# Kernel optimization log

Hardware: AMD Instinct MI355X
Metric: run time of the kernel (lower is better)

## Reference

```python
import jax, jax.numpy as jnp
import numpy as np
from jax import lax

EPS = 1e-12  # torch F.normalize eps


def _l2norm(x):
    n = jnp.linalg.norm(x, axis=-1, keepdims=True)
    return x / jnp.maximum(n, EPS)


def _conv1x1(x, w):
    # x: [B,C,H,W], w: [O,C] (1x1 conv, no bias)
    return jnp.einsum('bchw,oc->bohw', x, w)


def _se(x, w1, w2):
    # AdaptiveAvgPool2d(1) -> 1x1 conv (no bias) -> ReLU -> 1x1 conv (no bias) -> ReLU
    p = jnp.mean(x, axis=(2, 3))                      # [B,256]
    h = jax.nn.relu(jnp.einsum('bc,oc->bo', p, w1))   # [B,320]
    return jax.nn.relu(jnp.einsum('bc,oc->bo', h, w2))  # [B,1280]


def _tdec(x, wk_w, wk_b, wv_w, wv_b, red_w, rise_w, rise_b):
    # fc_reduce: 1x1 conv 256->128
    x1 = _conv1x1(x, red_w)                           # [B,128,H,W]
    B, d, H, W = x1.shape
    t = x1.reshape(B, d, H * W).transpose(0, 2, 1)    # [B,N,128] tokens
    # same WK linear produces both q and k (xq == xk in the source)
    k = _l2norm(jnp.einsum('bnd,ed->bne', t, wk_w) + wk_b)  # [B,N,128]
    v = _l2norm(jnp.einsum('bnd,ed->bne', t, wv_w) + wv_b)  # [B,N,128]
    # bmm(wq[B,d,N], wk[B,N,d]) -> [B,d,d] channel gram, temp 30 softmax
    attn = jax.nn.softmax(jnp.einsum('bni,bnj->bij', k, k) * 30.0, axis=-1)
    # bmm(attn[B,d,d], v^T[B,d,N]) -> [B,d,N], reshape back to map
    ot = jnp.einsum('bij,bnj->bin', attn, v).reshape(B, d, H, W)
    return _conv1x1(ot, rise_w) + rise_b[None, :, None, None]


def _fwd(x0, x1, x2, x3, x4, spec_w1, spec_w2, comm_w1, comm_w2,
         pre_w, pre_b, wk1_w, wk1_b, wv1_w, wv1_b, red1_w, rise1_w, rise1_b,
         wk2_w, wk2_b, wv2_w, wv2_b, red2_w, rise2_w, rise2_b):
    xs = jnp.stack([x0, x1, x2, x3, x4])              # [5,B,256,H,W]
    B = x0.shape[0]
    # reduce(lambda x,y: abs(x-y), down_x)
    diff = x0
    for xi in (x1, x2, x3, x4):
        diff = jnp.abs(diff - xi)
    ssum = xs.sum(axis=0)
    wd = jax.nn.softmax(_se(diff, spec_w1, spec_w2).reshape(B, 5, 256), axis=1)
    ws = jax.nn.softmax(_se(ssum, comm_w1, comm_w2).reshape(B, 5, 256), axis=1)
    # v2[i] = x_i*wd_i + x_i*ws_i + x_i ; v3 = sum_i v2[i]
    v3 = jnp.einsum('sbchw,bsc->bchw', xs, wd + ws + 1.0)
    pre = jax.nn.relu(
        lax.conv_general_dilated(v3, pre_w, (1, 1), ((1, 1), (1, 1)),
                                 dimension_numbers=('NCHW', 'OIHW', 'NCHW'))
        + pre_b[None, :, None, None])
    f1 = _tdec(pre, wk1_w, wk1_b, wv1_w, wv1_b, red1_w, rise1_w, rise1_b)
    f3 = _tdec(f1 + v3, wk2_w, wk2_b, wv2_w, wv2_b, red2_w, rise2_w, rise2_b)
    return f1 + f3 + v3


def setup_inputs() -> dict:
    key = jax.random.key(0)
    ks = iter(jax.random.split(key, 40))
    B, C, H, W = 16, 256, 64, 64

    def p(shape, scale=0.05):
        return jax.random.normal(next(ks), shape, jnp.float32) * scale

    inp = {f'x{i}': jax.random.normal(next(ks), (B, C, H, W), jnp.float32) for i in range(5)}
    inp.update(
        spec_w1=p((320, 256)), spec_w2=p((1280, 320)),
        comm_w1=p((320, 256)), comm_w2=p((1280, 320)),
        pre_w=p((256, 256, 3, 3)), pre_b=p((256,)),
        wk1_w=p((128, 128)), wk1_b=p((128,)), wv1_w=p((128, 128)), wv1_b=p((128,)),
        red1_w=p((128, 256)), rise1_w=p((256, 128)), rise1_b=p((256,)),
        wk2_w=p((128, 128)), wk2_b=p((128,)), wv2_w=p((128, 128)), wv2_b=p((128,)),
        red2_w=p((128, 256)), rise2_w=p((256, 128)), rise2_b=p((256,)),
    )
    return inp


def reference(x0, x1, x2, x3, x4, spec_w1, spec_w2, comm_w1, comm_w2,
              pre_w, pre_b, wk1_w, wk1_b, wv1_w, wv1_b, red1_w, rise1_w, rise1_b,
              wk2_w, wk2_b, wv2_w, wv2_b, red2_w, rise2_w, rise2_b):
    return _fwd(x0, x1, x2, x3, x4, spec_w1, spec_w2, comm_w1, comm_w2,
                pre_w, pre_b, wk1_w, wk1_b, wv1_w, wv1_b, red1_w, rise1_w, rise1_b,
                wk2_w, wk2_b, wv2_w, wv2_b, red2_w, rise2_w, rise2_b)
```

## Files before the change

### kernel.cpp

```cpp
#include <hip/hip_runtime.h>

#define DI __device__ __forceinline__

typedef short s16x8 __attribute__((ext_vector_type(8)));
typedef unsigned short u16;
typedef u16 u16x8 __attribute__((ext_vector_type(8)));
typedef u16 u16x16 __attribute__((ext_vector_type(16)));
typedef float f32x4 __attribute__((ext_vector_type(4)));

DI float bf2f(u16 v) { return __builtin_bit_cast(float, (unsigned)v << 16); }
DI u16 f2bf(float f) {
  unsigned u = __builtin_bit_cast(unsigned, f);
  return (u16)((u + 0x7fffu + ((u >> 16) & 1u)) >> 16);
}

__global__ void k_cast(u16* __restrict__ dst, const float* __restrict__ src, int n) {
  int i = blockIdx.x * 256 + threadIdx.x;
  if (i < n) dst[i] = f2bf(src[i]);
}

__global__ void k_wconv(u16* __restrict__ dst, const float* __restrict__ src) {
  int i = blockIdx.x * 256 + threadIdx.x;
  if (i < 9 * 256 * 256) {
    int tap = i >> 16, rem = i & 65535;
    dst[i] = f2bf(src[(size_t)rem * 9 + tap]);
  }
}

__global__ __launch_bounds__(256) void k_pool(
    const float* __restrict__ x0, const float* __restrict__ x1,
    const float* __restrict__ x2, const float* __restrict__ x3,
    const float* __restrict__ x4, float* __restrict__ pd, float* __restrict__ ps) {
  int c = blockIdx.x, b = blockIdx.y;
  size_t base = ((size_t)b * 256 + c) * 4096;
  float sd = 0.f, sm = 0.f;
  for (int p = threadIdx.x; p < 4096; p += 256) {
    float a0 = x0[base + p], a1 = x1[base + p], a2 = x2[base + p];
    float a3 = x3[base + p], a4 = x4[base + p];
    float d = fabsf(a0 - a1); d = fabsf(d - a2); d = fabsf(d - a3); d = fabsf(d - a4);
    sd += d; sm += a0 + a1 + a2 + a3 + a4;
  }
  for (int o = 32; o; o >>= 1) { sd += __shfl_xor(sd, o); sm += __shfl_xor(sm, o); }
  __shared__ float rb[4][2];
  int wv = threadIdx.x >> 6, lane = threadIdx.x & 63;
  if (!lane) { rb[wv][0] = sd; rb[wv][1] = sm; }
  __syncthreads();
  if (!threadIdx.x) {
    float a = rb[0][0] + rb[1][0] + rb[2][0] + rb[3][0];
    float s2 = rb[0][1] + rb[1][1] + rb[2][1] + rb[3][1];
    pd[b * 256 + c] = a * (1.f / 4096.f);
    ps[b * 256 + c] = s2 * (1.f / 4096.f);
  }
}

__global__ __launch_bounds__(256) void k_se1(
    const float* __restrict__ pd, const float* __restrict__ ps,
    const float* __restrict__ sw1, const float* __restrict__ cw1,
    float* __restrict__ h1) {
  int b = blockIdx.y, z = blockIdx.z;
  int wv = threadIdx.x >> 6, lane = threadIdx.x & 63;
  int e = blockIdx.x * 4 + wv;
  const float* in = (z ? ps : pd) + b * 256;
  const float* w = (z ? cw1 : sw1) + (size_t)e * 256;
  float a = 0.f;
#pragma unroll
  for (int i = 0; i < 4; ++i) a += in[lane + 64 * i] * w[lane + 64 * i];
  for (int o = 32; o; o >>= 1) a += __shfl_xor(a, o);
  if (!lane) h1[((size_t)z * 16 + b) * 320 + e] = fmaxf(a, 0.f);
}

__global__ __launch_bounds__(256) void k_se2(
    const float* __restrict__ h1, const float* __restrict__ sw2,
    const float* __restrict__ cw2, float* __restrict__ h2) {
  int b = blockIdx.y, z = blockIdx.z;
  int wv = threadIdx.x >> 6, lane = threadIdx.x & 63;
  int e = blockIdx.x * 4 + wv;
  const float* in = h1 + ((size_t)z * 16 + b) * 320;
  const float* w = (z ? cw2 : sw2) + (size_t)e * 320;
  float a = 0.f;
#pragma unroll
  for (int i = 0; i < 5; ++i) a += in[lane + 64 * i] * w[lane + 64 * i];
  for (int o = 32; o; o >>= 1) a += __shfl_xor(a, o);
  if (!lane) h2[((size_t)z * 16 + b) * 1280 + e] = fmaxf(a, 0.f);
}

__global__ __launch_bounds__(256) void k_se3(
    const float* __restrict__ h2, float* __restrict__ wt) {
  int b = blockIdx.x, t = threadIdx.x;
  const float* Hs = h2 + (size_t)b * 1280;
  const float* Hc = h2 + (size_t)(16 + b) * 1280;
  float d0 = Hs[t], d1 = Hs[256 + t], d2 = Hs[512 + t], d3 = Hs[768 + t], d4 = Hs[1024 + t];
  float m = fmaxf(fmaxf(fmaxf(d0, d1), fmaxf(d2, d3)), d4);
  float e0 = expf(d0 - m), e1 = expf(d1 - m), e2 = expf(d2 - m), e3 = expf(d3 - m), e4 = expf(d4 - m);
  float inv = 1.f / (e0 + e1 + e2 + e3 + e4);
  float c0 = Hc[t], c1 = Hc[256 + t], c2 = Hc[512 + t], c3 = Hc[768 + t], c4 = Hc[1024 + t];
  float mc = fmaxf(fmaxf(fmaxf(c0, c1), fmaxf(c2, c3)), c4);
  float g0 = expf(c0 - mc), g1 = expf(c1 - mc), g2 = expf(c2 - mc), g3 = expf(c3 - mc), g4 = expf(c4 - mc);
  float ci = 1.f / (g0 + g1 + g2 + g3 + g4);
  size_t base = (size_t)b * 1280 + t;
  wt[base + 0 * 256] = e0 * inv + g0 * ci + 1.f;
  wt[base + 1 * 256] = e1 * inv + g1 * ci + 1.f;
  wt[base + 2 * 256] = e2 * inv + g2 * ci + 1.f;
  wt[base + 3 * 256] = e3 * inv + g3 * ci + 1.f;
  wt[base + 4 * 256] = e4 * inv + g4 * ci + 1.f;
}

__global__ __launch_bounds__(256) void k_v3(
    const float* __restrict__ x0, const float* __restrict__ x1,
    const float* __restrict__ x2, const float* __restrict__ x3,
    const float* __restrict__ x4, const float* __restrict__ wt,
    u16* __restrict__ v3b) {
  int h = blockIdx.x, b = blockIdx.y;
  __shared__ float W[1280];
  for (int s = threadIdx.x; s < 1280; s += 256) W[s] = wt[(size_t)b * 1280 + s];
  __syncthreads();
  int t = threadIdx.x, w = t >> 2, oct = t & 3;
  size_t pbase = ((size_t)b * 256) * 4096 + h * 64 + w;
  size_t obase = ((size_t)b * 4096 + h * 64 + w) * 256;
  for (int pass = 0; pass < 8; ++pass) {
    int c0 = oct * 8 + pass * 32;
    u16x8 ov;
#pragma unroll
    for (int jj = 0; jj < 8; ++jj) {
      int c = c0 + jj;
      size_t a = pbase + (size_t)c * 4096;
      float s = x0[a] * W[c] + x1[a] * W[256 + c] + x2[a] * W[512 + c] +
                x3[a] * W[768 + c] + x4[a] * W[1024 + c];
      ov[jj] = f2bf(s);
    }
    *(u16x8*)(v3b + obase + c0) = ov;
  }
}

__global__ __launch_bounds__(256) void k_conv(
    const u16* __restrict__ v3b, const u16* __restrict__ Wt,
    const float* __restrict__ bias, u16* __restrict__ pre) {
  int o = blockIdx.x;
  int wg = (o & 7) * 128 + (o >> 3);
  int oh = wg & 1, hp = (wg >> 1) & 31, b = wg >> 6;
  __shared__ __align__(16) u16 Ain[4 * 66 * 40];
  __shared__ __align__(16) u16 Bld[2][128 * 40];
  int t = threadIdx.x, wv = t >> 6, lane = t & 63;
  int wm = (wv >> 1) * 64, wn = (wv & 1) * 64, fr = lane & 15, ko = lane >> 4;

  auto loadA = [&](int cc, int s) -> u16x16 {
    int r = s >> 7, rest = s & 127, w = rest >> 1, half = rest & 1;
    int hs = hp * 2 - 1 + r;
    u16x16 v = {};
    if ((unsigned)hs < 64u)
      v = *(const u16x16*)(v3b + (((size_t)b * 64 + hs) * 64 + w) * 256 + cc * 32 + half * 16);
    return v;
  };
  auto storeA = [&](int s, u16x16 v) {
    int r = s >> 7, rest = s & 127, w = rest >> 1, half = rest & 1;
    *(u16x16*)(Ain + (r * 66 + w + 1) * 40 + half * 16) = v;
  };
  auto loadB = [&](int tap, int cc) -> u16x16 {
    int n = t >> 1, half = t & 1;
    return *(const u16x16*)(Wt + ((size_t)tap * 256 + oh * 128 + n) * 256 + cc * 32 + half * 16);
  };
  auto storeB = [&](int bsel, u16x16 v) {
    int n = t >> 1, half = t & 1;
    *(u16x16*)(Bld[bsel] + n * 40 + half * 16) = v;
  };

  for (int s = t; s < 320; s += 256) {
    int r = s / 80, rem = s % 80;
    int col = (rem >= 40) ? 65 : 0, c = rem % 40;
    Ain[(r * 66 + col) * 40 + c] = 0;
  }
  storeA(t, loadA(0, t));
  storeA(t + 256, loadA(0, t + 256));
  storeB(0, loadB(0, 0));
  __syncthreads();

  f32x4 acc[4][4] = {};
  int buf = 0;
  for (int cc = 0; cc < 8; ++cc) {
#pragma unroll
    for (int tap = 0; tap < 9; ++tap) {
      u16x16 pA0, pA1, pB;
      bool doA = false, doB = false;
      if (tap < 8) {
        doB = true;
        pB = loadB(tap + 1, cc);
      } else if (cc < 7) {
        doA = true; doB = true;
        pB = loadB(0, cc + 1);
        pA0 = loadA(cc + 1, t);
        pA1 = loadA(cc + 1, t + 256);
      }
      const int dh = tap / 3 - 1, dw = tap % 3 - 1;
      s16x8 af[4], bfr[4];
#pragma unroll
      for (int i = 0; i < 4; ++i) {
        int m = wm + i * 16 + fr, r = m >> 6, wq = m & 63;
        af[i] = *(const s16x8*)(Ain + ((r + dh + 1) * 66 + (wq + dw + 1)) * 40 + ko * 8);
      }
#pragma unroll
      for (int j = 0; j < 4; ++j)
        bfr[j] = *(const s16x8*)(Bld[buf] + (wn + j * 16 + fr) * 40 + ko * 8);
#pragma unroll
      for (int i = 0; i < 4; ++i)
#pragma unroll
        for (int j = 0; j < 4; ++j)
          acc[i][j] = __builtin_amdgcn_mfma_f32_16x16x32_bf16(af[i], bfr[j], acc[i][j], 0, 0, 0);
      if (doA) __syncthreads();
      if (doB) storeB(buf ^ 1, pB);
      if (doA) { storeA(t, pA0); storeA(t + 256, pA1); }
      __syncthreads();
      buf ^= 1;
    }
  }
#pragma unroll
  for (int i = 0; i < 4; ++i) {
    int m0 = wm + i * 16 + ko * 4;
#pragma unroll
    for (int j = 0; j < 4; ++j) {
      int och = oh * 128 + wn + j * 16 + fr;
      float bv = bias[och];
#pragma unroll
      for (int r = 0; r < 4; ++r) {
        float v = fmaxf(acc[i][j][r] + bv, 0.f);
        pre[((size_t)b * 4096 + hp * 128 + m0 + r) * 256 + och] = f2bf(v);
      }
    }
  }
}

template <int MODE>
__global__ __launch_bounds__(256) void k_gemm(
    const u16* __restrict__ A, int lda, const u16* __restrict__ B0,
    const u16* __restrict__ B1, int ldb, int K,
    const float* __restrict__ bias0, const float* __restrict__ bias1,
    u16* __restrict__ out0, u16* __restrict__ out1,
    const u16* __restrict__ add0, const u16* __restrict__ add1,
    float* __restrict__ outf) {
  int nt = blockIdx.x, b = blockIdx.y, z = blockIdx.z;
  const u16* Ab = A + ((size_t)b * 4096 + nt * 128) * (size_t)lda;
  const u16* Bb;
  if constexpr (MODE == 1) Bb = (z ? B1 : B0);
  else if constexpr (MODE == 2) Bb = B0 + (size_t)b * 128 * ldb;
  else Bb = B0 + (size_t)z * 128 * ldb;
  __shared__ __align__(16) u16 Ald[128 * 40];
  __shared__ __align__(16) u16 Bld[128 * 40];
  int t = threadIdx.x, wv = t >> 6, lane = t & 63;
  int wm = (wv >> 1) * 64, wn = (wv & 1) * 64, fr = lane & 15, ko = lane >> 4;
  f32x4 acc[4][4] = {};
  for (int kc = 0; kc < K; kc += 32) {
    for (int s = t; s < 512; s += 256) {
      int r = s >> 2, ks = s & 3;
      *(u16x8*)(Ald + r * 40 + ks * 8) = *(const u16x8*)(Ab + (size_t)r * lda + kc + ks * 8);
    }
    for (int s = t; s < 512; s += 256) {
      int r = s >> 2, ks = s & 3;
      *(u16x8*)(Bld + r * 40 + ks * 8) = *(const u16x8*)(Bb + (size_t)r * ldb + kc + ks * 8);
    }
    __syncthreads();
    s16x8 af[4], bf[4];
#pragma unroll
    for (int i = 0; i < 4; ++i) af[i] = *(const s16x8*)(Ald + (wm + i * 16 + fr) * 40 + ko * 8);
#pragma unroll
    for (int j = 0; j < 4; ++j) bf[j] = *(const s16x8*)(Bld + (wn + j * 16 + fr) * 40 + ko * 8);
#pragma unroll
    for (int i = 0; i < 4; ++i)
#pragma unroll
      for (int j = 0; j < 4; ++j)
        acc[i][j] = __builtin_amdgcn_mfma_f32_16x16x32_bf16(af[i], bf[j], acc[i][j], 0, 0, 0);
    __syncthreads();
  }
  size_t tokbase = (size_t)b * 4096 + nt * 128;
#pragma unroll
  for (int i = 0; i < 4; ++i) {
    int m0 = wm + i * 16 + ko * 4;
#pragma unroll
    for (int j = 0; j < 4; ++j) {
      int nc = wn + j * 16 + fr;
      if constexpr (MODE == 0 || MODE == 2) {
        u16* dst = out0 + (tokbase + m0) * 128 + nc;
#pragma unroll
        for (int r = 0; r < 4; ++r) dst[(size_t)r * 128] = f2bf(acc[i][j][r]);
      } else if constexpr (MODE == 1) {
        float bv = (z ? bias1 : bias0)[nc];
        u16* dst = (z ? out1 : out0) + (tokbase + m0) * 128 + nc;
#pragma unroll
        for (int r = 0; r < 4; ++r) dst[(size_t)r * 128] = f2bf(acc[i][j][r] + bv);
      } else if constexpr (MODE == 3) {
        int o = z * 128 + nc;
        float bv = bias0[o];
        size_t idx = (tokbase + m0) * 256 + o;
#pragma unroll
        for (int r = 0; r < 4; ++r) {
          float f1v = acc[i][j][r] + bv;
          out0[idx + (size_t)r * 256] = f2bf(f1v);
          out1[idx + (size_t)r * 256] = f2bf(f1v + bf2f(add0[idx + (size_t)r * 256]));
        }
      } else {
        int o = z * 128 + nc;
        float bv = bias0[o];
        size_t idx = (tokbase + m0) * 256 + o;
        f32x4 vv;
#pragma unroll
        for (int r = 0; r < 4; ++r)
          vv[r] = acc[i][j][r] + bv + bf2f(add0[idx + (size_t)r * 256]) + bf2f(add1[idx + (size_t)r * 256]);
        *(f32x4*)(outf + ((size_t)b * 256 + o) * 4096 + nt * 128 + m0) = vv;
      }
    }
  }
}

__global__ __launch_bounds__(256) void k_norm(const u16* __restrict__ kraw,
                                              u16* __restrict__ ktout,
                                              u16* __restrict__ vbuf) {
  int nt = blockIdx.x, b = blockIdx.y, kind = blockIdx.z;
  int t = threadIdx.x, r = t >> 2, q = t & 3;
  __shared__ __align__(16) u16 T[128 * 72];
  size_t row = (size_t)b * 4096 + nt * 64 + r;
  const u16* src = (kind ? (const u16*)vbuf : kraw) + row * 128 + q * 32;
  float vals[32];
  float ss = 0.f;
#pragma unroll
  for (int s = 0; s < 4; ++s) {
    u16x8 v8 = *(const u16x8*)(src + s * 8);
#pragma unroll
    for (int e = 0; e < 8; ++e) { float f = bf2f(v8[e]); vals[s * 8 + e] = f; ss += f * f; }
  }
  ss += __shfl_xor(ss, 1);
  ss += __shfl_xor(ss, 2);
  float sc = 1.f / fmaxf(sqrtf(ss), 1e-12f);
  if (kind) {
    u16* dst = vbuf + row * 128 + q * 32;
#pragma unroll
    for (int s = 0; s < 4; ++s) {
      u16x8 o8;
#pragma unroll
      for (int e = 0; e < 8; ++e) o8[e] = f2bf(vals[s * 8 + e] * sc);
      *(u16x8*)(dst + s * 8) = o8;
    }
  } else {
#pragma unroll
    for (int s = 0; s < 4; ++s)
#pragma unroll
      for (int e = 0; e < 8; ++e)
        T[(q * 32 + s * 8 + e) * 72 + r] = f2bf(vals[s * 8 + e] * sc);
    __syncthreads();
    for (int s2 = t; s2 < 1024; s2 += 256) {
      int i = s2 >> 3, sg = s2 & 7;
      *(u16x8*)(ktout + ((size_t)b * 128 + i) * 4096 + nt * 64 + sg * 8) =
          *(const u16x8*)(T + i * 72 + sg * 8);
    }
  }
}

__global__ __launch_bounds__(256) void k_gram(const u16* __restrict__ kt, float* __restrict__ gp) {
  int ks = blockIdx.x, b = blockIdx.y;
  const u16* base = kt + (size_t)b * 128 * 4096 + ks * 256;
  __shared__ __align__(16) u16 Tld[128 * 40];
  int t = threadIdx.x, wv = t >> 6, lane = t & 63;
  int wm = (wv >> 1) * 64, wn = (wv & 1) * 64, fr = lane & 15, ko = lane >> 4;
  f32x4 acc[4][4] = {};
  for (int kc = 0; kc < 256; kc += 32) {
    for (int s = t; s < 512; s += 256) {
      int r = s >> 2, k2 = s & 3;
      *(u16x8*)(Tld + r * 40 + k2 * 8) = *(const u16x8*)(base + (size_t)r * 4096 + kc + k2 * 8);
    }
    __syncthreads();
    s16x8 af[4], bf[4];
#pragma unroll
    for (int i = 0; i < 4; ++i) af[i] = *(const s16x8*)(Tld + (wm + i * 16 + fr) * 40 + ko * 8);
#pragma unroll
    for (int j = 0; j < 4; ++j) bf[j] = *(const s16x8*)(Tld + (wn + j * 16 + fr) * 40 + ko * 8);
#pragma unroll
    for (int i = 0; i < 4; ++i)
#pragma unroll
      for (int j = 0; j < 4; ++j)
        acc[i][j] = __builtin_amdgcn_mfma_f32_16x16x32_bf16(af[i], bf[j], acc[i][j], 0, 0, 0);
    __syncthreads();
  }
  float* dst = gp + ((size_t)(ks * 16 + b) * 128) * 128;
#pragma unroll
  for (int i = 0; i < 4; ++i) {
    int m0 = wm + i * 16 + ko * 4;
#pragma unroll
    for (int j = 0; j < 4; ++j) {
      int nc = wn + j * 16 + fr;
#pragma unroll
      for (int r = 0; r < 4; ++r) dst[(size_t)(m0 + r) * 128 + nc] = acc[i][j][r];
    }
  }
}

__global__ void k_soft(const float* __restrict__ gp, u16* __restrict__ attn) {
  int i = blockIdx.x, b = blockIdx.y, l = threadIdx.x;
  float s0 = 0.f, s1 = 0.f;
  for (int ks = 0; ks < 16; ++ks) {
    const float* row = gp + (((size_t)ks * 16 + b) * 128 + i) * 128;
    s0 += row[l]; s1 += row[l + 64];
  }
  s0 *= 30.f; s1 *= 30.f;
  float m = fmaxf(s0, s1);
  for (int o = 32; o; o >>= 1) m = fmaxf(m, __shfl_xor(m, o));
  float e0 = expf(s0 - m), e1 = expf(s1 - m);
  float s = e0 + e1;
  for (int o = 32; o; o >>= 1) s += __shfl_xor(s, o);
  float inv = 1.f / s;
  u16* dst = attn + ((size_t)b * 128 + i) * 128;
  dst[l] = f2bf(e0 * inv);
  dst[l + 64] = f2bf(e1 * inv);
}

extern "C" void kernel_launch(void* const* d_in, const int* in_sizes, int n_in,
                              void* d_out, int out_size, void* d_ws, size_t ws_size,
                              hipStream_t stream) {
  (void)in_sizes; (void)n_in; (void)out_size; (void)ws_size;
  const float* x0 = (const float*)d_in[0];
  const float* x1 = (const float*)d_in[1];
  const float* x2 = (const float*)d_in[2];
  const float* x3 = (const float*)d_in[3];
  const float* x4 = (const float*)d_in[4];
  const float* spec_w1 = (const float*)d_in[5];
  const float* spec_w2 = (const float*)d_in[6];
  const float* comm_w1 = (const float*)d_in[7];
  const float* comm_w2 = (const float*)d_in[8];
  const float* pre_w = (const float*)d_in[9];
  const float* pre_bias = (const float*)d_in[10];
  const float* wk1_w = (const float*)d_in[11];
  const float* wk1_b = (const float*)d_in[12];
  const float* wv1_w = (const float*)d_in[13];
  const float* wv1_b = (const float*)d_in[14];
  const float* red1_w = (const float*)d_in[15];
  const float* rise1_w = (const float*)d_in[16];
  const float* rise1_b = (const float*)d_in[17];
  const float* wk2_w = (const float*)d_in[18];
  const float* wk2_b = (const float*)d_in[19];
  const float* wv2_w = (const float*)d_in[20];
  const float* wv2_b = (const float*)d_in[21];
  const float* red2_w = (const float*)d_in[22];
  const float* rise2_w = (const float*)d_in[23];
  const float* rise2_b = (const float*)d_in[24];
  float* out = (float*)d_out;

  char* wsp = (char*)d_ws;
  size_t off = 0;
  auto alloc = [&](size_t bytes) -> void* {
    off = (off + 255) & ~(size_t)255;
    void* p = wsp + off;
    off += bytes;
    return p;
  };
  float* pd = (float*)alloc(16 * 256 * 4);
  float* ps = (float*)alloc(16 * 256 * 4);
  float* h1b = (float*)alloc(2 * 16 * 320 * 4);
  float* h2b = (float*)alloc(2 * 16 * 1280 * 4);
  float* wtb = (float*)alloc(16 * 5 * 256 * 4);
  u16* v3b = (u16*)alloc((size_t)16 * 4096 * 256 * 2);
  u16* Wtc = (u16*)alloc((size_t)9 * 256 * 256 * 2);
  u16* red1b = (u16*)alloc(128 * 256 * 2);
  u16* wk1b = (u16*)alloc(128 * 128 * 2);
  u16* wv1b = (u16*)alloc(128 * 128 * 2);
  u16* rise1b = (u16*)alloc(256 * 128 * 2);
  u16* red2b = (u16*)alloc(128 * 256 * 2);
  u16* wk2b = (u16*)alloc(128 * 128 * 2);
  u16* wv2b = (u16*)alloc(128 * 128 * 2);
  u16* rise2b = (u16*)alloc(256 * 128 * 2);
  u16* pre = (u16*)alloc((size_t)16 * 4096 * 256 * 2);
  u16* tbuf = (u16*)alloc((size_t)16 * 4096 * 128 * 2);
  u16* kraw = (u16*)alloc((size_t)16 * 4096 * 128 * 2);
  u16* khat = (u16*)alloc((size_t)16 * 4096 * 128 * 2);
  u16* vbuf = (u16*)alloc((size_t)16 * 4096 * 128 * 2);
  u16* attn = (u16*)alloc((size_t)16 * 128 * 128 * 2);
  u16* Obuf = (u16*)alloc((size_t)16 * 4096 * 128 * 2);
  u16* f1b = (u16*)alloc((size_t)16 * 4096 * 256 * 2);
  float* gpart = (float*)tbuf;
  u16* in2b = pre;

  k_cast<<<dim3(128), 256, 0, stream>>>(red1b, red1_w, 32768);
  k_cast<<<dim3(64), 256, 0, stream>>>(wk1b, wk1_w, 16384);
  k_cast<<<dim3(64), 256, 0, stream>>>(wv1b, wv1_w, 16384);
  k_cast<<<dim3(128), 256, 0, stream>>>(rise1b, rise1_w, 32768);
  k_cast<<<dim3(128), 256, 0, stream>>>(red2b, red2_w, 32768);
  k_cast<<<dim3(64), 256, 0, stream>>>(wk2b, wk2_w, 16384);
  k_cast<<<dim3(64), 256, 0, stream>>>(wv2b, wv2_w, 16384);
  k_cast<<<dim3(128), 256, 0, stream>>>(rise2b, rise2_w, 32768);
  k_wconv<<<dim3(2304), 256, 0, stream>>>(Wtc, pre_w);

  k_pool<<<dim3(256, 16), 256, 0, stream>>>(x0, x1, x2, x3, x4, pd, ps);
  k_se1<<<dim3(80, 16, 2), 256, 0, stream>>>(pd, ps, spec_w1, comm_w1, h1b);
  k_se2<<<dim3(320, 16, 2), 256, 0, stream>>>(h1b, spec_w2, comm_w2, h2b);
  k_se3<<<dim3(16), 256, 0, stream>>>(h2b, wtb);
  k_v3<<<dim3(64, 16), 256, 0, stream>>>(x0, x1, x2, x3, x4, wtb, v3b);
  k_conv<<<dim3(1024), 256, 0, stream>>>(v3b, Wtc, pre_bias, pre);

  k_gemm<0><<<dim3(32, 16, 1), 256, 0, stream>>>(pre, 256, red1b, nullptr, 256, 256,
      nullptr, nullptr, tbuf, nullptr, nullptr, nullptr, nullptr);
  k_gemm<1><<<dim3(32, 16, 2), 256, 0, stream>>>(tbuf, 128, wk1b, wv1b, 128, 128,
      wk1_b, wv1_b, kraw, vbuf, nullptr, nullptr, nullptr);
  k_norm<<<dim3(64, 16, 2), 256, 0, stream>>>(kraw, khat, vbuf);
  k_gram<<<dim3(16, 16), 256, 0, stream>>>(khat, gpart);
  k_soft<<<dim3(128, 16), 64, 0, stream>>>(gpart, attn);
  k_gemm<2><<<dim3(32, 16, 1), 256, 0, stream>>>(vbuf, 128, attn, nullptr, 128, 128,
      nullptr, nullptr, Obuf, nullptr, nullptr, nullptr, nullptr);
  k_gemm<3><<<dim3(32, 16, 2), 256, 0, stream>>>(Obuf, 128, rise1b, nullptr, 128, 128,
      rise1_b, nullptr, f1b, in2b, v3b, nullptr, nullptr);

  k_gemm<0><<<dim3(32, 16, 1), 256, 0, stream>>>(in2b, 256, red2b, nullptr, 256, 256,
      nullptr, nullptr, tbuf, nullptr, nullptr, nullptr, nullptr);
  k_gemm<1><<<dim3(32, 16, 2), 256, 0, stream>>>(tbuf, 128, wk2b, wv2b, 128, 128,
      wk2_b, wv2_b, kraw, vbuf, nullptr, nullptr, nullptr);
  k_norm<<<dim3(64, 16, 2), 256, 0, stream>>>(kraw, khat, vbuf);
  k_gram<<<dim3(16, 16), 256, 0, stream>>>(khat, gpart);
  k_soft<<<dim3(128, 16), 64, 0, stream>>>(gpart, attn);
  k_gemm<2><<<dim3(32, 16, 1), 256, 0, stream>>>(vbuf, 128, attn, nullptr, 128, 128,
      nullptr, nullptr, Obuf, nullptr, nullptr, nullptr, nullptr);
  k_gemm<4><<<dim3(32, 16, 2), 256, 0, stream>>>(Obuf, 128, rise2b, nullptr, 128, 128,
      rise2_b, nullptr, nullptr, nullptr, f1b, v3b, out);
}
```

Before: 536.6 us.

## Fuse reduce, QKV projection and L2-norm into one kernel; restage v3 transpose

Replaces the separate reduce GEMM, K/V projection GEMM and normalisation kernels with one k_qkv kernel. It keeps the reduced tokens in shared memory, applies the bias and L2 norm in registers, and writes khat already transposed. This removes the round trips of tbuf and kraw through global memory and two launches per attention block. Separately, k_v3 now reads the inputs coalesced along width and transposes through shared memory, and the eight weight-cast launches are merged into one. The fused kernel uses more shared memory and issues its K and V projections serially inside each block, with grid size 32x16 instead of 32x16x2.

```diff
diff --git a/kernel.cpp b/kernel.cpp
--- a/kernel.cpp
+++ b/kernel.cpp
@@ -14,9 +14,22 @@
   return (u16)((u + 0x7fffu + ((u >> 16) & 1u)) >> 16);
 }
 
-__global__ void k_cast(u16* __restrict__ dst, const float* __restrict__ src, int n) {
+__global__ void k_cast8(u16* __restrict__ dst,
+    const float* __restrict__ s0, const float* __restrict__ s1,
+    const float* __restrict__ s2, const float* __restrict__ s3,
+    const float* __restrict__ s4, const float* __restrict__ s5,
+    const float* __restrict__ s6, const float* __restrict__ s7) {
   int i = blockIdx.x * 256 + threadIdx.x;
-  if (i < n) dst[i] = f2bf(src[i]);
+  const float* src; int base;
+  if (i < 32768) { src = s0; base = 0; }
+  else if (i < 49152) { src = s1; base = 32768; }
+  else if (i < 65536) { src = s2; base = 49152; }
+  else if (i < 98304) { src = s3; base = 65536; }
+  else if (i < 131072) { src = s4; base = 98304; }
+  else if (i < 147456) { src = s5; base = 131072; }
+  else if (i < 163840) { src = s6; base = 147456; }
+  else { src = s7; base = 163840; }
+  dst[i] = f2bf(src[i - base]);
 }
 
 __global__ void k_wconv(u16* __restrict__ dst, const float* __restrict__ src) {
@@ -112,22 +125,27 @@
     u16* __restrict__ v3b) {
   int h = blockIdx.x, b = blockIdx.y;
   __shared__ float W[1280];
-  for (int s = threadIdx.x; s < 1280; s += 256) W[s] = wt[(size_t)b * 1280 + s];
+  __shared__ u16 T[256][72];
+  int t = threadIdx.x, wv = t >> 6, l = t & 63;
+  for (int s = t; s < 1280; s += 256) W[s] = wt[(size_t)b * 1280 + s];
   __syncthreads();
-  int t = threadIdx.x, w = t >> 2, oct = t & 3;
-  size_t pbase = ((size_t)b * 256) * 4096 + h * 64 + w;
+  size_t rowbase = (size_t)b * 256 * 4096 + h * 64 + l;
+#pragma unroll 4
+  for (int k = 0; k < 64; ++k) {
+    int c = wv * 64 + k;
+    size_t a = rowbase + (size_t)c * 4096;
+    float s = x0[a] * W[c] + x1[a] * W[256 + c] + x2[a] * W[512 + c] +
+              x3[a] * W[768 + c] + x4[a] * W[1024 + c];
+    T[c][l] = f2bf(s);
+  }
+  __syncthreads();
+  int w = t >> 2, oct = t & 3;
   size_t obase = ((size_t)b * 4096 + h * 64 + w) * 256;
   for (int pass = 0; pass < 8; ++pass) {
     int c0 = oct * 8 + pass * 32;
     u16x8 ov;
 #pragma unroll
-    for (int jj = 0; jj < 8; ++jj) {
-      int c = c0 + jj;
-      size_t a = pbase + (size_t)c * 4096;
-      float s = x0[a] * W[c] + x1[a] * W[256 + c] + x2[a] * W[512 + c] +
-                x3[a] * W[768 + c] + x4[a] * W[1024 + c];
-      ov[jj] = f2bf(s);
-    }
+    for (int jj = 0; jj < 8; ++jj) ov[jj] = T[c0 + jj][w];
     *(u16x8*)(v3b + obase + c0) = ov;
   }
 }
@@ -228,6 +246,159 @@
   }
 }
 
+__global__ __launch_bounds__(256) void k_qkv(
+    const u16* __restrict__ in,
+    const u16* __restrict__ redW,
+    const u16* __restrict__ wkW,
+    const u16* __restrict__ wvW,
+    const float* __restrict__ kb, const float* __restrict__ vb,
+    u16* __restrict__ vout,
+    u16* __restrict__ khat) {
+  int nt = blockIdx.x, b = blockIdx.y;
+  const u16* Ab = in + ((size_t)b * 4096 + nt * 128) * 256;
+  __shared__ __align__(16) u16 Ald[128 * 40];
+  __shared__ __align__(16) u16 Bld[128 * 40];
+  __shared__ __align__(16) u16 T[128 * 136];
+  __shared__ float SS[2][128];
+  int t = threadIdx.x, wv = t >> 6, lane = t & 63;
+  int wm = (wv >> 1) * 64, wn = (wv & 1) * 64, fr = lane & 15, ko = lane >> 4;
+  f32x4 acc[4][4] = {};
+  for (int kc = 0; kc < 256; kc += 32) {
+    for (int s = t; s < 512; s += 256) {
+      int r = s >> 2, ks = s & 3;
+      *(u16x8*)(Ald + r * 40 + ks * 8) = *(const u16x8*)(Ab + (size_t)r * 256 + kc + ks * 8);
+    }
+    for (int s = t; s < 512; s += 256) {
+      int r = s >> 2, ks = s & 3;
+      *(u16x8*)(Bld + r * 40 + ks * 8) = *(const u16x8*)(redW + (size_t)r * 256 + kc + ks * 8);
+    }
+    __syncthreads();
+    s16x8 af[4], bf[4];
+#pragma unroll
+    for (int i = 0; i < 4; ++i) af[i] = *(const s16x8*)(Ald + (wm + i * 16 + fr) * 40 + ko * 8);
+#pragma unroll
+    for (int j = 0; j < 4; ++j) bf[j] = *(const s16x8*)(Bld + (wn + j * 16 + fr) * 40 + ko * 8);
+#pragma unroll
+    for (int i = 0; i < 4; ++i)
+#pragma unroll
+      for (int j = 0; j < 4; ++j)
+        acc[i][j] = __builtin_amdgcn_mfma_f32_16x16x32_bf16(af[i], bf[j], acc[i][j], 0, 0, 0);
+    __syncthreads();
+  }
+#pragma unroll
+  for (int i = 0; i < 4; ++i)
+#pragma unroll
+    for (int j = 0; j < 4; ++j)
+#pragma unroll
+      for (int r = 0; r < 4; ++r)
+        T[(wm + i * 16 + ko * 4 + r) * 136 + wn + j * 16 + fr] = f2bf(acc[i][j][r]);
+
+  for (int z = 0; z < 2; ++z) {
+    const u16* W = z ? wkW : wvW;
+    const float* bias = z ? kb : vb;
+    f32x4 a2[4][4] = {};
+#pragma unroll
+    for (int h = 0; h < 2; ++h) {
+      __syncthreads();
+      for (int s = t; s < 512; s += 256) {
+        int r = s >> 2, ks = s & 3;
+        *(u16x8*)(Ald + r * 40 + ks * 8) = *(const u16x8*)(W + (size_t)r * 128 + h * 64 + ks * 8);
+      }
+      for (int s = t; s < 512; s += 256) {
+        int r = s >> 2, ks = s & 3;
+        *(u16x8*)(Bld + r * 40 + ks * 8) = *(const u16x8*)(W + (size_t)r * 128 + h * 64 + 32 + ks * 8);
+      }
+      __syncthreads();
+#pragma unroll
+      for (int kk = 0; kk < 2; ++kk) {
+        const u16* Bsrc = kk ? Bld : Ald;
+        s16x8 af[4], bf[4];
+#pragma unroll
+        for (int i = 0; i < 4; ++i)
+          af[i] = *(const s16x8*)(T + (size_t)(wm + i * 16 + fr) * 136 + h * 64 + kk * 32 + ko * 8);
+#pragma unroll
+        for (int j = 0; j < 4; ++j)
+          bf[j] = *(const s16x8*)(Bsrc + (wn + j * 16 + fr) * 40 + ko * 8);
+#pragma unroll
+        for (int i = 0; i < 4; ++i)
+#pragma unroll
+          for (int j = 0; j < 4; ++j)
+            a2[i][j] = __builtin_amdgcn_mfma_f32_16x16x32_bf16(af[i], bf[j], a2[i][j], 0, 0, 0);
+      }
+    }
+    float bj[4];
+#pragma unroll
+    for (int j = 0; j < 4; ++j) bj[j] = bias[wn + j * 16 + fr];
+    float pss[4][4];
+#pragma unroll
+    for (int i = 0; i < 4; ++i)
+#pragma unroll
+      for (int r = 0; r < 4; ++r) pss[i][r] = 0.f;
+#pragma unroll
+    for (int i = 0; i < 4; ++i)
+#pragma unroll
+      for (int j = 0; j < 4; ++j)
+#pragma unroll
+        for (int r = 0; r < 4; ++r) {
+          float v = a2[i][j][r] + bj[j];
+          a2[i][j][r] = v;
+          pss[i][r] += v * v;
+        }
+#pragma unroll
+    for (int m = 1; m < 16; m <<= 1)
+#pragma unroll
+      for (int i = 0; i < 4; ++i)
+#pragma unroll
+        for (int r = 0; r < 4; ++r) pss[i][r] += __shfl_xor(pss[i][r], m);
+    if (fr == 0)
+#pragma unroll
+      for (int i = 0; i < 4; ++i)
+#pragma unroll
+        for (int r = 0; r < 4; ++r) SS[wv & 1][wm + i * 16 + ko * 4 + r] = pss[i][r];
+    __syncthreads();
+    float sc[4][4];
+#pragma unroll
+    for (int i = 0; i < 4; ++i)
+#pragma unroll
+      for (int r = 0; r < 4; ++r) {
+        int tok = wm + i * 16 + ko * 4 + r;
+        float s2 = SS[0][tok] + SS[1][tok];
+        sc[i][r] = 1.f / fmaxf(sqrtf(s2), 1e-12f);
+      }
+#pragma unroll
+    for (int i = 0; i < 4; ++i)
+#pragma unroll
+      for (int j = 0; j < 4; ++j)
+#pragma unroll
+        for (int r = 0; r < 4; ++r) a2[i][j][r] *= sc[i][r];
+    if (z == 0) {
+      size_t tokbase = (size_t)b * 4096 + nt * 128;
+#pragma unroll
+      for (int i = 0; i < 4; ++i)
+#pragma unroll
+        for (int j = 0; j < 4; ++j) {
+          u16* dst = vout + (tokbase + wm + i * 16 + ko * 4) * 128 + wn + j * 16 + fr;
+#pragma unroll
+          for (int r = 0; r < 4; ++r) dst[(size_t)r * 128] = f2bf(a2[i][j][r]);
+        }
+    } else {
+#pragma unroll
+      for (int i = 0; i < 4; ++i)
+#pragma unroll
+        for (int j = 0; j < 4; ++j)
+#pragma unroll
+          for (int r = 0; r < 4; ++r)
+            T[(size_t)(wn + j * 16 + fr) * 136 + wm + i * 16 + ko * 4 + r] = f2bf(a2[i][j][r]);
+      __syncthreads();
+      for (int s = t; s < 2048; s += 256) {
+        int ch = s >> 4, sg = s & 15;
+        *(u16x8*)(khat + ((size_t)b * 128 + ch) * 4096 + nt * 128 + sg * 8) =
+            *(const u16x8*)(T + ch * 136 + sg * 8);
+      }
+    }
+  }
+}
+
 template <int MODE>
 __global__ __launch_bounds__(256) void k_gemm(
     const u16* __restrict__ A, int lda, const u16* __restrict__ B0,
@@ -239,8 +410,7 @@
   int nt = blockIdx.x, b = blockIdx.y, z = blockIdx.z;
   const u16* Ab = A + ((size_t)b * 4096 + nt * 128) * (size_t)lda;
   const u16* Bb;
-  if constexpr (MODE == 1) Bb = (z ? B1 : B0);
-  else if constexpr (MODE == 2) Bb = B0 + (size_t)b * 128 * ldb;
+  if constexpr (MODE == 2) Bb = B0 + (size_t)b * 128 * ldb;
   else Bb = B0 + (size_t)z * 128 * ldb;
   __shared__ __align__(16) u16 Ald[128 * 40];
   __shared__ __align__(16) u16 Bld[128 * 40];
@@ -276,15 +446,10 @@
 #pragma unroll
     for (int j = 0; j < 4; ++j) {
       int nc = wn + j * 16 + fr;
-      if constexpr (MODE == 0 || MODE == 2) {
+      if constexpr (MODE == 2) {
         u16* dst = out0 + (tokbase + m0) * 128 + nc;
 #pragma unroll
         for (int r = 0; r < 4; ++r) dst[(size_t)r * 128] = f2bf(acc[i][j][r]);
-      } else if constexpr (MODE == 1) {
-        float bv = (z ? bias1 : bias0)[nc];
-        u16* dst = (z ? out1 : out0) + (tokbase + m0) * 128 + nc;
-#pragma unroll
-        for (int r = 0; r < 4; ++r) dst[(size_t)r * 128] = f2bf(acc[i][j][r] + bv);
       } else if constexpr (MODE == 3) {
         int o = z * 128 + nc;
         float bv = bias0[o];
@@ -305,49 +470,6 @@
           vv[r] = acc[i][j][r] + bv + bf2f(add0[idx + (size_t)r * 256]) + bf2f(add1[idx + (size_t)r * 256]);
         *(f32x4*)(outf + ((size_t)b * 256 + o) * 4096 + nt * 128 + m0) = vv;
       }
-    }
-  }
-}
-
-__global__ __launch_bounds__(256) void k_norm(const u16* __restrict__ kraw,
-                                              u16* __restrict__ ktout,
-                                              u16* __restrict__ vbuf) {
-  int nt = blockIdx.x, b = blockIdx.y, kind = blockIdx.z;
-  int t = threadIdx.x, r = t >> 2, q = t & 3;
-  __shared__ __align__(16) u16 T[128 * 72];
-  size_t row = (size_t)b * 4096 + nt * 64 + r;
-  const u16* src = (kind ? (const u16*)vbuf : kraw) + row * 128 + q * 32;
-  float vals[32];
-  float ss = 0.f;
-#pragma unroll
-  for (int s = 0; s < 4; ++s) {
-    u16x8 v8 = *(const u16x8*)(src + s * 8);
-#pragma unroll
-    for (int e = 0; e < 8; ++e) { float f = bf2f(v8[e]); vals[s * 8 + e] = f; ss += f * f; }
-  }
-  ss += __shfl_xor(ss, 1);
-  ss += __shfl_xor(ss, 2);
-  float sc = 1.f / fmaxf(sqrtf(ss), 1e-12f);
-  if (kind) {
-    u16* dst = vbuf + row * 128 + q * 32;
-#pragma unroll
-    for (int s = 0; s < 4; ++s) {
-      u16x8 o8;
-#pragma unroll
-      for (int e = 0; e < 8; ++e) o8[e] = f2bf(vals[s * 8 + e] * sc);
-      *(u16x8*)(dst + s * 8) = o8;
-    }
-  } else {
-#pragma unroll
-    for (int s = 0; s < 4; ++s)
-#pragma unroll
-      for (int e = 0; e < 8; ++e)
-        T[(q * 32 + s * 8 + e) * 72 + r] = f2bf(vals[s * 8 + e] * sc);
-    __syncthreads();
-    for (int s2 = t; s2 < 1024; s2 += 256) {
-      int i = s2 >> 3, sg = s2 & 7;
-      *(u16x8*)(ktout + ((size_t)b * 128 + i) * 4096 + nt * 64 + sg * 8) =
-          *(const u16x8*)(T + i * 72 + sg * 8);
     }
   }
 }
@@ -455,17 +577,17 @@
   float* wtb = (float*)alloc(16 * 5 * 256 * 4);
   u16* v3b = (u16*)alloc((size_t)16 * 4096 * 256 * 2);
   u16* Wtc = (u16*)alloc((size_t)9 * 256 * 256 * 2);
-  u16* red1b = (u16*)alloc(128 * 256 * 2);
-  u16* wk1b = (u16*)alloc(128 * 128 * 2);
-  u16* wv1b = (u16*)alloc(128 * 128 * 2);
-  u16* rise1b = (u16*)alloc(256 * 128 * 2);
-  u16* red2b = (u16*)alloc(128 * 256 * 2);
-  u16* wk2b = (u16*)alloc(128 * 128 * 2);
-  u16* wv2b = (u16*)alloc(128 * 128 * 2);
-  u16* rise2b = (u16*)alloc(256 * 128 * 2);
+  u16* wall = (u16*)alloc((size_t)196608 * 2);
+  u16* red1b = wall;
+  u16* wk1b = wall + 32768;
+  u16* wv1b = wall + 49152;
+  u16* rise1b = wall + 65536;
+  u16* red2b = wall + 98304;
+  u16* wk2b = wall + 131072;
+  u16* wv2b = wall + 147456;
+  u16* rise2b = wall + 163840;
   u16* pre = (u16*)alloc((size_t)16 * 4096 * 256 * 2);
   u16* tbuf = (u16*)alloc((size_t)16 * 4096 * 128 * 2);
-  u16* kraw = (u16*)alloc((size_t)16 * 4096 * 128 * 2);
   u16* khat = (u16*)alloc((size_t)16 * 4096 * 128 * 2);
   u16* vbuf = (u16*)alloc((size_t)16 * 4096 * 128 * 2);
   u16* attn = (u16*)alloc((size_t)16 * 128 * 128 * 2);
@@ -474,14 +596,8 @@
   float* gpart = (float*)tbuf;
   u16* in2b = pre;
 
-  k_cast<<<dim3(128), 256, 0, stream>>>(red1b, red1_w, 32768);
-  k_cast<<<dim3(64), 256, 0, stream>>>(wk1b, wk1_w, 16384);
-  k_cast<<<dim3(64), 256, 0, stream>>>(wv1b, wv1_w, 16384);
-  k_cast<<<dim3(128), 256, 0, stream>>>(rise1b, rise1_w, 32768);
-  k_cast<<<dim3(128), 256, 0, stream>>>(red2b, red2_w, 32768);
-  k_cast<<<dim3(64), 256, 0, stream>>>(wk2b, wk2_w, 16384);
-  k_cast<<<dim3(64), 256, 0, stream>>>(wv2b, wv2_w, 16384);
-  k_cast<<<dim3(128), 256, 0, stream>>>(rise2b, rise2_w, 32768);
+  k_cast8<<<dim3(768), 256, 0, stream>>>(wall, red1_w, wk1_w, wv1_w, rise1_w,
+                                         red2_w, wk2_w, wv2_w, rise2_w);
   k_wconv<<<dim3(2304), 256, 0, stream>>>(Wtc, pre_w);
 
   k_pool<<<dim3(256, 16), 256, 0, stream>>>(x0, x1, x2, x3, x4, pd, ps);
@@ -491,11 +607,7 @@
   k_v3<<<dim3(64, 16), 256, 0, stream>>>(x0, x1, x2, x3, x4, wtb, v3b);
   k_conv<<<dim3(1024), 256, 0, stream>>>(v3b, Wtc, pre_bias, pre);
 
-  k_gemm<0><<<dim3(32, 16, 1), 256, 0, stream>>>(pre, 256, red1b, nullptr, 256, 256,
-      nullptr, nullptr, tbuf, nullptr, nullptr, nullptr, nullptr);
-  k_gemm<1><<<dim3(32, 16, 2), 256, 0, stream>>>(tbuf, 128, wk1b, wv1b, 128, 128,
-      wk1_b, wv1_b, kraw, vbuf, nullptr, nullptr, nullptr);
-  k_norm<<<dim3(64, 16, 2), 256, 0, stream>>>(kraw, khat, vbuf);
+  k_qkv<<<dim3(32, 16), 256, 0, stream>>>(pre, red1b, wk1b, wv1b, wk1_b, wv1_b, vbuf, khat);
   k_gram<<<dim3(16, 16), 256, 0, stream>>>(khat, gpart);
   k_soft<<<dim3(128, 16), 64, 0, stream>>>(gpart, attn);
   k_gemm<2><<<dim3(32, 16, 1), 256, 0, stream>>>(vbuf, 128, attn, nullptr, 128, 128,
@@ -503,11 +615,7 @@
   k_gemm<3><<<dim3(32, 16, 2), 256, 0, stream>>>(Obuf, 128, rise1b, nullptr, 128, 128,
       rise1_b, nullptr, f1b, in2b, v3b, nullptr, nullptr);
 
-  k_gemm<0><<<dim3(32, 16, 1), 256, 0, stream>>>(in2b, 256, red2b, nullptr, 256, 256,
-      nullptr, nullptr, tbuf, nullptr, nullptr, nullptr, nullptr);
-  k_gemm<1><<<dim3(32, 16, 2), 256, 0, stream>>>(tbuf, 128, wk2b, wv2b, 128, 128,
-      wk2_b, wv2_b, kraw, vbuf, nullptr, nullptr, nullptr);
-  k_norm<<<dim3(64, 16, 2), 256, 0, stream>>>(kraw, khat, vbuf);
+  k_qkv<<<dim3(32, 16), 256, 0, stream>>>(in2b, red2b, wk2b, wv2b, wk2_b, wv2_b, vbuf, khat);
   k_gram<<<dim3(16, 16), 256, 0, stream>>>(khat, gpart);
   k_soft<<<dim3(128, 16), 64, 0, stream>>>(gpart, attn);
   k_gemm<2><<<dim3(32, 16, 1), 256, 0, stream>>>(vbuf, 128, attn, nullptr, 128, 128,
```

After: 494.5 us. 1.09x faster.
